# Optimization experiments

Hardware: AMD Instinct MI355X
Metric: run time of the kernel (lower is better)

The kernel has to match this reference:

```python
import jax, jax.numpy as jnp
import numpy as np

B, S, D = 512, 199, 128
PRO, SKILL = 20000, 500


def setup_inputs() -> dict:
    key = jax.random.key(0)
    ks = jax.random.split(key, 32)
    rn = lambda k, shape: jax.random.normal(k, shape, dtype=jnp.float32) * 0.05
    inp = {}
    inp["last_problem"] = jax.random.randint(ks[0], (B, S), 0, PRO, dtype=jnp.int32)
    inp["last_skill"] = jax.random.randint(ks[1], (B, S), 0, SKILL, dtype=jnp.int32)
    inp["last_ans"] = jax.random.randint(ks[2], (B, S), 0, 2, dtype=jnp.int32)
    inp["next_problem"] = jax.random.randint(ks[3], (B, S), 0, PRO, dtype=jnp.int32)
    inp["next_skill"] = jax.random.randint(ks[4], (B, S), 0, SKILL, dtype=jnp.int32)
    inp["next_ans"] = jax.random.randint(ks[5], (B, S), 0, 2, dtype=jnp.int32)
    inp["pro_embed"] = rn(ks[6], (PRO, D))
    inp["skill_embed"] = rn(ks[7], (SKILL, D))
    inp["ans_embed"] = rn(ks[8], (2, D))
    inp["time_embed"] = rn(ks[9], (200, D))
    inp["ls_state"] = rn(ks[10], (1, D))
    inp["pro_state0"] = rn(ks[11], (199, D))
    inp["skill_state0"] = rn(ks[12], (199, D))
    inp["akt_pro_diff"] = rn(ks[13], (PRO, 1))
    inp["akt_pro_change"] = rn(ks[14], (SKILL, D))
    # Linear weights stored as [in, out] (torch W.T); biases zero-init.
    inp["W_pf"] = rn(ks[15], (2 * D, D)); inp["b_pf"] = jnp.zeros((D,), jnp.float32)
    inp["W_sf"] = rn(ks[16], (2 * D, D)); inp["b_sf"] = jnp.zeros((D,), jnp.float32)
    inp["W_af"] = rn(ks[17], (2 * D, D)); inp["b_af"] = jnp.zeros((D,), jnp.float32)
    inp["W_ps"] = rn(ks[18], (2 * D, D)); inp["b_ps"] = jnp.zeros((D,), jnp.float32)
    inp["W_ss"] = rn(ks[19], (2 * D, D)); inp["b_ss"] = jnp.zeros((D,), jnp.float32)
    inp["W_as"] = rn(ks[20], (2 * D, D)); inp["b_as"] = jnp.zeros((D,), jnp.float32)
    inp["W_o1"] = rn(ks[21], (4 * D, D)); inp["b_o1"] = jnp.zeros((D,), jnp.float32)
    inp["W_o2"] = rn(ks[22], (D, 1));     inp["b_o2"] = jnp.zeros((1,), jnp.float32)
    return inp


def _forward(next_problem, next_skill, next_ans,
             pro_embed, skill_embed, ans_embed, time_embed, ls_state,
             pro_state0, skill_state0, akt_pro_diff, akt_pro_change,
             W_pf, b_pf, W_sf, b_sf, W_af, b_af,
             W_ps, b_ps, W_ss, b_ss, W_as, b_as,
             W_o1, b_o1, W_o2, b_o2):
    Bb, Ss = next_problem.shape
    Dd = pro_embed.shape[1]
    # [B,S,D] question embedding with AKT-style difficulty modulation
    npe = (pro_embed[next_problem] + skill_embed[next_skill]
           + akt_pro_diff[next_problem] * akt_pro_change[next_skill])
    nX = npe + ans_embed[next_ans]
    atge = time_embed[1]  # all_time_gap == 1 every step
    bidx = jnp.arange(Bb)

    def step(carry, x):
        pro_state, skill_state, all_state, lpt_tab, lst_tab = carry
        t, npe_t, nX_t, pidx, sidx = x
        # gather last-seen states via per-batch time indices
        lpt = lpt_tab[bidx, pidx]               # [B] int
        lbp = pro_state[bidx, lpt]              # [B,D]
        tge = time_embed[t - lpt]               # [B,D]
        lst = lst_tab[bidx, sidx]
        lbs = skill_state[bidx, lst]
        stge = time_embed[t - lst]
        # forget gates
        lbp = lbp * jax.nn.sigmoid(jnp.concatenate([lbp, tge], -1) @ W_pf + b_pf)
        lbs = lbs * jax.nn.sigmoid(jnp.concatenate([lbs, stge], -1) @ W_sf + b_sf)
        atge_b = jnp.broadcast_to(atge, all_state.shape)
        la = all_state * jax.nn.sigmoid(jnp.concatenate([all_state, atge_b], -1) @ W_af + b_af)
        # prediction head
        final = jnp.concatenate([la, lbp, lbs, npe_t], -1)  # [B,4D]
        P = jax.nn.sigmoid(jax.nn.relu(final @ W_o1 + b_o1) @ W_o2 + b_o2)[:, 0]
        # state updates
        new_all = la + jnp.tanh(jnp.concatenate([la, nX_t], -1) @ W_as + b_as)
        new_pro = lbp + jnp.tanh(jnp.concatenate([lbp, nX_t], -1) @ W_ps + b_ps)
        new_skill = lbs + jnp.tanh(jnp.concatenate([lbs, nX_t], -1) @ W_ss + b_ss)
        # scatter time and state back
        lpt_tab = lpt_tab.at[bidx, pidx].set(t)
        lst_tab = lst_tab.at[bidx, sidx].set(t)
        pro_state = jax.lax.dynamic_update_slice_in_dim(pro_state, new_pro[:, None, :], t, axis=1)
        skill_state = jax.lax.dynamic_update_slice_in_dim(skill_state, new_skill[:, None, :], t, axis=1)
        return (pro_state, skill_state, new_all, lpt_tab, lst_tab), P

    init = (jnp.broadcast_to(pro_state0[None], (Bb, pro_state0.shape[0], Dd)),
            jnp.broadcast_to(skill_state0[None], (Bb, skill_state0.shape[0], Dd)),
            jnp.broadcast_to(ls_state, (Bb, Dd)),
            jnp.zeros((Bb, akt_pro_diff.shape[0]), jnp.int32),
            jnp.zeros((Bb, akt_pro_change.shape[0]), jnp.int32))
    xs = (jnp.arange(Ss, dtype=jnp.int32),
          jnp.swapaxes(npe, 0, 1), jnp.swapaxes(nX, 0, 1),
          next_problem.T, next_skill.T)
    _, Ps = jax.lax.scan(step, init, xs)  # Ps: [S,B]
    return Ps.T  # [B,S]


def reference(last_problem, last_skill, last_ans, next_problem, next_skill, next_ans,
              pro_embed, skill_embed, ans_embed, time_embed, ls_state,
              pro_state0, skill_state0, akt_pro_diff, akt_pro_change,
              W_pf, b_pf, W_sf, b_sf, W_af, b_af,
              W_ps, b_ps, W_ss, b_ss, W_as, b_as,
              W_o1, b_o1, W_o2, b_o2):
    # last_problem/last_skill/last_ans are only used for shape in the original forward
    return _forward(next_problem, next_skill, next_ans,
                    pro_embed, skill_embed, ans_embed, time_embed, ls_state,
                    pro_state0, skill_state0, akt_pro_diff, akt_pro_change,
                    W_pf, b_pf, W_sf, b_sf, W_af, b_af,
                    W_ps, b_ps, W_ss, b_ss, W_as, b_as,
                    W_o1, b_o1, W_o2, b_o2)
```

## Files before the change

kernel.cpp:

```cpp
#include <hip/hip_runtime.h>
#include <hip/hip_bf16.h>

typedef __bf16 bf16;
typedef bf16 bf16x8 __attribute__((ext_vector_type(8)));
typedef bf16 bf16x4 __attribute__((ext_vector_type(4)));
typedef float f32x4 __attribute__((ext_vector_type(4)));
typedef unsigned int u32;
typedef unsigned short u16;

#define Bsz 512
#define Ssz 199
#define Dsz 128
#define GR 16
#define NBLK (Bsz / GR)
#define BTot (Bsz * Ssz)

__device__ __forceinline__ float fsig(float x) {
  return __builtin_amdgcn_rcpf(1.f + __builtin_amdgcn_exp2f(x * -1.44269504f));
}
__device__ __forceinline__ float ftanh(float x) {
  return 1.f - 2.f * __builtin_amdgcn_rcpf(1.f + __builtin_amdgcn_exp2f(x * 2.88539008f));
}
__device__ __forceinline__ f32x4 mfma16(bf16x8 a, bf16x8 b, f32x4 c) {
  return __builtin_amdgcn_mfma_f32_16x16x32_bf16(a, b, c, 0, 0, 0);
}
__device__ __forceinline__ bf16x8 ldfrag(const bf16* PW, int KS, int nt, int ks, int lane) {
  return *(const bf16x8*)&PW[(size_t)((nt * KS + ks) * 64 + lane) * 8];
}
__device__ __forceinline__ void keep(bf16x8& v) {
  f32x4& f = reinterpret_cast<f32x4&>(v);
  asm volatile("" : "+v"(f));
}
__device__ __forceinline__ void barL() {
  __builtin_amdgcn_sched_barrier(0);
  asm volatile("s_waitcnt lgkmcnt(0)" ::: "memory");
  __builtin_amdgcn_s_barrier();
  __builtin_amdgcn_sched_barrier(0);
}

__global__ void k_idx(const int* __restrict__ np_, const int* __restrict__ ns_,
                      u32* __restrict__ idx) {
  __shared__ u16 tabP[20000];
  __shared__ u16 tabS[500];
  __shared__ u16 pb[Ssz], sb[Ssz];
  int b = blockIdx.x;
  for (int i = threadIdx.x; i < 20000; i += blockDim.x) tabP[i] = 0;
  for (int i = threadIdx.x; i < 500; i += blockDim.x) tabS[i] = 0;
  for (int i = threadIdx.x; i < Ssz; i += blockDim.x) {
    pb[i] = (u16)np_[b * Ssz + i];
    sb[i] = (u16)ns_[b * Ssz + i];
  }
  __syncthreads();
  if (threadIdx.x == 0) {
    for (int t = 0; t < Ssz; ++t) {
      int p = pb[t], s = sb[t];
      idx[b * Ssz + t] = (u32)tabP[p] | ((u32)tabS[s] << 8);
      tabP[p] = (u16)t;
      tabS[s] = (u16)t;
    }
  }
}

__global__ void k_pack(const float* __restrict__ W, bf16* __restrict__ dst, int K) {
  int g = blockIdx.x * blockDim.x + threadIdx.x;
  int KS = K / 32;
  int total = 8 * KS * 64;
  if (g >= total) return;
  int l = g & 63;
  int ks = (g >> 6) % KS;
  int nt = (g >> 6) / KS;
  int col = nt * 16 + (l & 15);
  int k0 = ks * 32 + (l >> 4) * 8;
  bf16x8 v;
  for (int j = 0; j < 8; ++j) v[j] = (bf16)W[(size_t)(k0 + j) * 128 + col];
  *(bf16x8*)&dst[(size_t)g * 8] = v;
}

__global__ void k_tge(const float* __restrict__ TE, const float* __restrict__ W,
                      const float* __restrict__ bias, float* __restrict__ dst) {
  __shared__ float te[128];
  int d = blockIdx.x, n = threadIdx.x;
  te[n] = TE[d * 128 + n];
  __syncthreads();
  float acc = bias[n];
  for (int k = 0; k < 128; ++k) acc += te[k] * W[(size_t)(128 + k) * 128 + n];
  dst[d * 128 + n] = acc;
}

__global__ void k_embed(const int* __restrict__ np_, const int* __restrict__ ns_,
                        const int* __restrict__ na_,
                        const float* __restrict__ pe, const float* __restrict__ se,
                        const float* __restrict__ diff, const float* __restrict__ chg,
                        const float* __restrict__ ae, bf16* __restrict__ nXsS) {
  int g = blockIdx.x * 256 + threadIdx.x;
  int bt = g >> 5, cg = (g & 31) * 4;
  if (bt >= BTot) return;
  int b = bt / Ssz, t = bt - b * Ssz;
  int p = np_[bt], s = ns_[bt], a = na_[bt];
  float d = diff[p];
  f32x4 vp = *(const f32x4*)&pe[(size_t)p * 128 + cg];
  f32x4 vs = *(const f32x4*)&se[(size_t)s * 128 + cg];
  f32x4 vc = *(const f32x4*)&chg[(size_t)s * 128 + cg];
  f32x4 va = *(const f32x4*)&ae[(size_t)a * 128 + cg];
  bf16x4 ox;
  for (int j = 0; j < 4; ++j) ox[j] = (bf16)(vp[j] + vs[j] + d * vc[j] + va[j]);
  *(bf16x4*)&nXsS[((size_t)t * Bsz + b) * 128 + cg] = ox;
}

struct MainParams {
  const float *ls_state, *pro_state0, *skill_state0;
  const u32 *idx;
  const bf16 *nXsS;
  const float *TGEp, *TGEs, *cAF;
  const bf16 *PWpf, *PWsf, *PWaf, *PWps, *PWss, *PWas;
  const float *b_ps, *b_ss, *b_as;
  bf16 *proSt, *skSt, *Sla, *Slbp, *Slbs;
};

__global__ void __launch_bounds__(512) k_main(MainParams P) {
  const int b0 = blockIdx.x * GR;
  const int tid = threadIdx.x;
  const int lane = tid & 63;
  const int wv = tid >> 6;
  const int r32 = tid >> 5;
  const int c4 = (tid & 31) * 4;
  const int arow = lane & 15, apos = (lane >> 4) * 8;
  const int rb = (lane >> 4) * 4;
  const int cA = wv * 16 + (lane & 15);

  __shared__ __align__(16) bf16 Ala[16][136], Albp[16][136], Albs[16][136], AnX[16][136];
  __shared__ __align__(16) bf16 STG0[16][132], STG1[16][132], STGa[16][132];
  __shared__ u32 idxL[GR * Ssz];

  bf16x8 Wpf[4], Wsf[4], Waf[4], Wps[8], Wss[8], Was[8];
#pragma unroll
  for (int ks = 0; ks < 4; ++ks) {
    Wpf[ks] = ldfrag(P.PWpf, 4, wv, ks, lane);
    Wsf[ks] = ldfrag(P.PWsf, 4, wv, ks, lane);
    Waf[ks] = ldfrag(P.PWaf, 4, wv, ks, lane);
  }
#pragma unroll
  for (int ks = 0; ks < 8; ++ks) {
    Wps[ks] = ldfrag(P.PWps, 8, wv, ks, lane);
    Wss[ks] = ldfrag(P.PWss, 8, wv, ks, lane);
    Was[ks] = ldfrag(P.PWas, 8, wv, ks, lane);
  }
#pragma unroll
  for (int ks = 0; ks < 4; ++ks) {
    keep(Wpf[ks]);
    keep(Wsf[ks]);
    keep(Waf[ks]);
  }
#pragma unroll
  for (int ks = 0; ks < 8; ++ks) {
    keep(Wps[ks]);
    keep(Wss[ks]);
    keep(Was[ks]);
  }
  const float bpsv = P.b_ps[cA], bssv = P.b_ss[cA], basv = P.b_as[cA], cafv = P.cAF[cA];

  for (int i = tid; i < GR * Ssz; i += 512) idxL[i] = P.idx[b0 * Ssz + i];
  __syncthreads();

  float gpc[4], gsc[4];
  {
    bf16x4 va, vp, vs;
    for (int j = 0; j < 4; ++j) {
      va[j] = (bf16)P.ls_state[c4 + j];
      vp[j] = (bf16)P.pro_state0[c4 + j];
      vs[j] = (bf16)P.skill_state0[c4 + j];
    }
    *(bf16x4*)&Ala[r32][c4] = va;
    *(bf16x4*)&Albp[r32][c4] = vp;
    *(bf16x4*)&Albs[r32][c4] = vs;
    *(bf16x4*)&AnX[r32][c4] = *(const bf16x4*)&P.nXsS[(size_t)(b0 + r32) * Dsz + c4];
#pragma unroll
    for (int r = 0; r < 4; ++r) {
      gpc[r] = P.TGEp[cA];
      gsc[r] = P.TGEs[cA];
    }
  }
  __syncthreads();

  for (int t = 0; t < Ssz; ++t) {
    const bool pf = (t + 1 < Ssz);
    float gpn[4], gsn[4];
    bf16x4 pPro{}, pSk{}, pNxs{};
    u32 iwN = 0;
    if (pf) {
#pragma unroll
      for (int r = 0; r < 4; ++r) {
        u32 iw = idxL[(rb + r) * Ssz + t + 1];
        int lp = iw & 255, ls = (iw >> 8) & 255;
        gpn[r] = P.TGEp[(size_t)(t + 1 - lp) * Dsz + cA];
        gsn[r] = P.TGEs[(size_t)(t + 1 - ls) * Dsz + cA];
      }
      iwN = idxL[r32 * Ssz + t + 1];
      int lpN = iwN & 255, lsN = (iwN >> 8) & 255;
      if (lpN != t)
        pPro = *(const bf16x4*)&P.proSt[((size_t)(b0 + r32) * Ssz + lpN) * Dsz + c4];
      if (lsN != t)
        pSk = *(const bf16x4*)&P.skSt[((size_t)(b0 + r32) * Ssz + lsN) * Dsz + c4];
      pNxs = *(const bf16x4*)&P.nXsS[((size_t)(t + 1) * Bsz + (b0 + r32)) * Dsz + c4];
    }
    f32x4 dpf = {gpc[0], gpc[1], gpc[2], gpc[3]};
    f32x4 dsf = {gsc[0], gsc[1], gsc[2], gsc[3]};
    f32x4 daf = {cafv, cafv, cafv, cafv};
#pragma unroll
    for (int ks = 0; ks < 4; ++ks) {
      bf16x8 ap = *(const bf16x8*)&Albp[arow][ks * 32 + apos];
      bf16x8 av = *(const bf16x8*)&Albs[arow][ks * 32 + apos];
      bf16x8 aa = *(const bf16x8*)&Ala[arow][ks * 32 + apos];
      dpf = mfma16(ap, Wpf[ks], dpf);
      dsf = mfma16(av, Wsf[ks], dsf);
      daf = mfma16(aa, Waf[ks], daf);
    }
    barL();
    float gP[4], gS[4], gA[4];
#pragma unroll
    for (int r = 0; r < 4; ++r) {
      int row = rb + r;
      float sp = (float)Albp[row][cA];
      float gv = sp * fsig(dpf[r]);
      gP[r] = gv;
      Albp[row][cA] = (bf16)gv;
      float ss = (float)Albs[row][cA];
      float gw = ss * fsig(dsf[r]);
      gS[r] = gw;
      Albs[row][cA] = (bf16)gw;
      float sa = (float)Ala[row][cA];
      float gx = sa * fsig(daf[r]);
      gA[r] = gx;
      Ala[row][cA] = (bf16)gx;
    }
    barL();
    {
      size_t db = ((size_t)(b0 + r32) * Ssz + t) * Dsz + c4;
      *(bf16x4*)&P.Sla[db] = *(const bf16x4*)&Ala[r32][c4];
      *(bf16x4*)&P.Slbp[db] = *(const bf16x4*)&Albp[r32][c4];
      *(bf16x4*)&P.Slbs[db] = *(const bf16x4*)&Albs[r32][c4];
    }
    f32x4 uas{}, ups{}, uss{};
#pragma unroll
    for (int ks = 0; ks < 4; ++ks) {
      bf16x8 aa = *(const bf16x8*)&Ala[arow][ks * 32 + apos];
      bf16x8 ap = *(const bf16x8*)&Albp[arow][ks * 32 + apos];
      bf16x8 av = *(const bf16x8*)&Albs[arow][ks * 32 + apos];
      bf16x8 ax = *(const bf16x8*)&AnX[arow][ks * 32 + apos];
      uas = mfma16(aa, Was[ks], uas);
      uas = mfma16(ax, Was[ks + 4], uas);
      ups = mfma16(ap, Wps[ks], ups);
      ups = mfma16(ax, Wps[ks + 4], ups);
      uss = mfma16(av, Wss[ks], uss);
      uss = mfma16(ax, Wss[ks + 4], uss);
    }
#pragma unroll
    for (int r = 0; r < 4; ++r) {
      int row = rb + r;
      STG0[row][cA] = (bf16)(gP[r] + ftanh(ups[r] + bpsv));
      STG1[row][cA] = (bf16)(gS[r] + ftanh(uss[r] + bssv));
      STGa[row][cA] = (bf16)(gA[r] + ftanh(uas[r] + basv));
    }
    barL();
    {
      size_t base = ((size_t)(b0 + r32) * Ssz + t) * Dsz + c4;
      bf16x4 npv = *(const bf16x4*)&STG0[r32][c4];
      bf16x4 nsv = *(const bf16x4*)&STG1[r32][c4];
      *(bf16x4*)&P.proSt[base] = npv;
      *(bf16x4*)&P.skSt[base] = nsv;
      if (pf) {
        int lpN = iwN & 255, lsN = (iwN >> 8) & 255;
        *(bf16x4*)&Ala[r32][c4] = *(const bf16x4*)&STGa[r32][c4];
        *(bf16x4*)&Albp[r32][c4] = (lpN == t) ? npv : pPro;
        *(bf16x4*)&Albs[r32][c4] = (lsN == t) ? nsv : pSk;
        *(bf16x4*)&AnX[r32][c4] = pNxs;
#pragma unroll
        for (int r = 0; r < 4; ++r) {
          gpc[r] = gpn[r];
          gsc[r] = gsn[r];
        }
      }
    }
    __syncthreads();
  }
}

struct HeadParams {
  const bf16 *Sla, *Slbp, *Slbs, *PWo1;
  const int *next_problem, *next_skill;
  const float *pro_embed, *skill_embed, *akt_pro_diff, *akt_pro_change;
  const float *b_o1, *W_o2, *b_o2;
  float *out;
};

__global__ void k_head(HeadParams P) {
  const int bt0 = blockIdx.x * 32;
  const int tid = threadIdx.x, lane = tid & 63, wv = tid >> 6;
  const int r16 = tid >> 4, c8 = (tid & 15) * 8;
  const int arow = lane & 15, apos = (lane >> 4) * 8;
  const int rb = (lane >> 4) * 4;
  const int nt0 = wv, nt1 = wv + 4;
  const int cAh = nt0 * 16 + (lane & 15), cBh = nt1 * 16 + (lane & 15);
  __shared__ __align__(16) bf16 Af[32][520];
  __shared__ float Hh[32][132];
  __shared__ float Hpart[32][16];
  __shared__ float w2s[128];
  if (tid < 128) w2s[tid] = P.W_o2[tid];
  for (int half = 0; half < 2; ++half) {
    int row = half * 16 + r16;
    int bt = bt0 + row;
    *(bf16x8*)&Af[row][c8] = *(const bf16x8*)&P.Sla[(size_t)bt * 128 + c8];
    *(bf16x8*)&Af[row][128 + c8] = *(const bf16x8*)&P.Slbp[(size_t)bt * 128 + c8];
    *(bf16x8*)&Af[row][256 + c8] = *(const bf16x8*)&P.Slbs[(size_t)bt * 128 + c8];
    int np = P.next_problem[bt], ns = P.next_skill[bt];
    float diff = P.akt_pro_diff[np];
    f32x4 p0 = *(const f32x4*)&P.pro_embed[(size_t)np * 128 + c8];
    f32x4 p1 = *(const f32x4*)&P.pro_embed[(size_t)np * 128 + c8 + 4];
    f32x4 s0 = *(const f32x4*)&P.skill_embed[(size_t)ns * 128 + c8];
    f32x4 s1 = *(const f32x4*)&P.skill_embed[(size_t)ns * 128 + c8 + 4];
    f32x4 c0 = *(const f32x4*)&P.akt_pro_change[(size_t)ns * 128 + c8];
    f32x4 c1 = *(const f32x4*)&P.akt_pro_change[(size_t)ns * 128 + c8 + 4];
    bf16x8 vn;
    for (int j = 0; j < 4; ++j) {
      vn[j] = (bf16)(p0[j] + s0[j] + diff * c0[j]);
      vn[j + 4] = (bf16)(p1[j] + s1[j] + diff * c1[j]);
    }
    *(bf16x8*)&Af[row][384 + c8] = vn;
  }
  __syncthreads();
  f32x4 h0{}, h1{}, h2{}, h3{};
#pragma unroll
  for (int ks = 0; ks < 16; ++ks) {
    bf16x8 a0 = *(const bf16x8*)&Af[arow][ks * 32 + apos];
    bf16x8 a1 = *(const bf16x8*)&Af[16 + arow][ks * 32 + apos];
    bf16x8 bA = ldfrag(P.PWo1, 16, nt0, ks, lane);
    bf16x8 bB = ldfrag(P.PWo1, 16, nt1, ks, lane);
    h0 = mfma16(a0, bA, h0);
    h1 = mfma16(a0, bB, h1);
    h2 = mfma16(a1, bA, h2);
    h3 = mfma16(a1, bB, h3);
  }
  const float bo1A = P.b_o1[cAh], bo1B = P.b_o1[cBh];
  for (int r = 0; r < 4; ++r) {
    Hh[rb + r][cAh] = fmaxf(h0[r] + bo1A, 0.f);
    Hh[rb + r][cBh] = fmaxf(h1[r] + bo1B, 0.f);
    Hh[16 + rb + r][cAh] = fmaxf(h2[r] + bo1A, 0.f);
    Hh[16 + rb + r][cBh] = fmaxf(h3[r] + bo1B, 0.f);
  }
  __syncthreads();
  for (int half = 0; half < 2; ++half) {
    int row = half * 16 + (tid >> 4), cg = tid & 15;
    float s = 0.f;
#pragma unroll
    for (int j = 0; j < 8; ++j) s += Hh[row][cg * 8 + j] * w2s[cg * 8 + j];
    Hpart[row][cg] = s;
  }
  __syncthreads();
  if (tid < 32) {
    float s = 0.f;
#pragma unroll
    for (int k = 0; k < 16; ++k) s += Hpart[tid][k];
    P.out[bt0 + tid] = fsig(s + P.b_o2[0]);
  }
}

extern "C" void kernel_launch(void* const* d_in, const int* in_sizes, int n_in,
                              void* d_out, int out_size, void* d_ws, size_t ws_size,
                              hipStream_t stream) {
  const int* next_problem = (const int*)d_in[3];
  const int* next_skill = (const int*)d_in[4];
  const int* next_ans = (const int*)d_in[5];
  const float* pro_embed = (const float*)d_in[6];
  const float* skill_embed = (const float*)d_in[7];
  const float* ans_embed = (const float*)d_in[8];
  const float* time_embed = (const float*)d_in[9];
  const float* ls_state = (const float*)d_in[10];
  const float* pro_state0 = (const float*)d_in[11];
  const float* skill_state0 = (const float*)d_in[12];
  const float* akt_pro_diff = (const float*)d_in[13];
  const float* akt_pro_change = (const float*)d_in[14];
  const float* W_pf = (const float*)d_in[15];
  const float* b_pf = (const float*)d_in[16];
  const float* W_sf = (const float*)d_in[17];
  const float* b_sf = (const float*)d_in[18];
  const float* W_af = (const float*)d_in[19];
  const float* b_af = (const float*)d_in[20];
  const float* W_ps = (const float*)d_in[21];
  const float* b_ps = (const float*)d_in[22];
  const float* W_ss = (const float*)d_in[23];
  const float* b_ss = (const float*)d_in[24];
  const float* W_as = (const float*)d_in[25];
  const float* b_as = (const float*)d_in[26];
  const float* W_o1 = (const float*)d_in[27];
  const float* b_o1 = (const float*)d_in[28];
  const float* W_o2 = (const float*)d_in[29];
  const float* b_o2 = (const float*)d_in[30];

  char* ws = (char*)d_ws;
  size_t off = 0;
  auto alloc = [&](size_t bytes) -> void* {
    void* p = ws + off;
    off += bytes;
    off = (off + 255) & ~(size_t)255;
    return p;
  };
  bf16* proSt = (bf16*)alloc((size_t)Bsz * Ssz * Dsz * 2);
  bf16* skSt = (bf16*)alloc((size_t)Bsz * Ssz * Dsz * 2);
  u32* idx = (u32*)alloc((size_t)BTot * 4);
  float* TGEp = (float*)alloc(200 * 128 * 4);
  float* TGEs = (float*)alloc(200 * 128 * 4);
  float* cAF = (float*)alloc(128 * 4);
  bf16* PWpf = (bf16*)alloc(128 * 128 * 2);
  bf16* PWsf = (bf16*)alloc(128 * 128 * 2);
  bf16* PWaf = (bf16*)alloc(128 * 128 * 2);
  bf16* PWps = (bf16*)alloc(256 * 128 * 2);
  bf16* PWss = (bf16*)alloc(256 * 128 * 2);
  bf16* PWas = (bf16*)alloc(256 * 128 * 2);
  bf16* PWo1 = (bf16*)alloc(512 * 128 * 2);
  bf16* nXsS = (bf16*)alloc((size_t)BTot * Dsz * 2);
  bf16* Sla = (bf16*)alloc((size_t)BTot * Dsz * 2);
  bf16* Slbp = (bf16*)alloc((size_t)BTot * Dsz * 2);
  bf16* Slbs = (bf16*)alloc((size_t)BTot * Dsz * 2);

  if (off > ws_size) {
    hipMemsetAsync(d_out, 0xFF, (size_t)out_size * 4, stream);
    return;
  }

  k_idx<<<Bsz, 256, 0, stream>>>(next_problem, next_skill, idx);
  k_pack<<<8, 256, 0, stream>>>(W_pf, PWpf, 128);
  k_pack<<<8, 256, 0, stream>>>(W_sf, PWsf, 128);
  k_pack<<<8, 256, 0, stream>>>(W_af, PWaf, 128);
  k_pack<<<16, 256, 0, stream>>>(W_ps, PWps, 256);
  k_pack<<<16, 256, 0, stream>>>(W_ss, PWss, 256);
  k_pack<<<16, 256, 0, stream>>>(W_as, PWas, 256);
  k_pack<<<32, 256, 0, stream>>>(W_o1, PWo1, 512);
  k_tge<<<200, 128, 0, stream>>>(time_embed, W_pf, b_pf, TGEp);
  k_tge<<<200, 128, 0, stream>>>(time_embed, W_sf, b_sf, TGEs);
  k_tge<<<1, 128, 0, stream>>>(time_embed + 128, W_af, b_af, cAF);
  k_embed<<<(BTot * 32 + 255) / 256, 256, 0, stream>>>(
      next_problem, next_skill, next_ans, pro_embed, skill_embed, akt_pro_diff,
      akt_pro_change, ans_embed, nXsS);

  MainParams mp;
  mp.ls_state = ls_state; mp.pro_state0 = pro_state0; mp.skill_state0 = skill_state0;
  mp.idx = idx;
  mp.nXsS = nXsS;
  mp.TGEp = TGEp; mp.TGEs = TGEs; mp.cAF = cAF;
  mp.PWpf = PWpf; mp.PWsf = PWsf; mp.PWaf = PWaf;
  mp.PWps = PWps; mp.PWss = PWss; mp.PWas = PWas;
  mp.b_ps = b_ps; mp.b_ss = b_ss; mp.b_as = b_as;
  mp.proSt = proSt; mp.skSt = skSt;
  mp.Sla = Sla; mp.Slbp = Slbp; mp.Slbs = Slbs;

  k_main<<<NBLK, 512, 0, stream>>>(mp);

  HeadParams hp;
  hp.Sla = Sla; hp.Slbp = Slbp; hp.Slbs = Slbs; hp.PWo1 = PWo1;
  hp.next_problem = next_problem; hp.next_skill = next_skill;
  hp.pro_embed = pro_embed; hp.skill_embed = skill_embed;
  hp.akt_pro_diff = akt_pro_diff; hp.akt_pro_change = akt_pro_change;
  hp.b_o1 = b_o1; hp.W_o2 = W_o2; hp.b_o2 = b_o2;
  hp.out = (float*)d_out;
  k_head<<<BTot / 32, 256, 0, stream>>>(hp);
}
```

Measured before the change: 715.7 us.

## Double-buffer recurrent state in LDS and defer global stores by one step

```diff
diff --git a/kernel.cpp b/kernel.cpp
--- a/kernel.cpp
+++ b/kernel.cpp
@@ -128,8 +128,9 @@
   const int rb = (lane >> 4) * 4;
   const int cA = wv * 16 + (lane & 15);
 
-  __shared__ __align__(16) bf16 Ala[16][136], Albp[16][136], Albs[16][136], AnX[16][136];
-  __shared__ __align__(16) bf16 STG0[16][132], STG1[16][132], STGa[16][132];
+  __shared__ __align__(16) bf16 Ala[2][16][136], Albp[2][16][136], Albs[2][16][136];
+  __shared__ __align__(16) bf16 AnX[2][16][136];
+  __shared__ __align__(16) bf16 STG0[2][16][132], STG1[2][16][132], STGa[16][132];
   __shared__ u32 idxL[GR * Ssz];
 
   bf16x8 Wpf[4], Wsf[4], Waf[4], Wps[8], Wss[8], Was[8];
@@ -170,10 +171,10 @@
       vp[j] = (bf16)P.pro_state0[c4 + j];
       vs[j] = (bf16)P.skill_state0[c4 + j];
     }
-    *(bf16x4*)&Ala[r32][c4] = va;
-    *(bf16x4*)&Albp[r32][c4] = vp;
-    *(bf16x4*)&Albs[r32][c4] = vs;
-    *(bf16x4*)&AnX[r32][c4] = *(const bf16x4*)&P.nXsS[(size_t)(b0 + r32) * Dsz + c4];
+    *(bf16x4*)&Ala[0][r32][c4] = va;
+    *(bf16x4*)&Albp[0][r32][c4] = vp;
+    *(bf16x4*)&Albs[0][r32][c4] = vs;
+    *(bf16x4*)&AnX[0][r32][c4] = *(const bf16x4*)&P.nXsS[(size_t)(b0 + r32) * Dsz + c4];
 #pragma unroll
     for (int r = 0; r < 4; ++r) {
       gpc[r] = P.TGEp[cA];
@@ -184,9 +185,18 @@
 
   for (int t = 0; t < Ssz; ++t) {
     const bool pf = (t + 1 < Ssz);
+    const int cur = t & 1, prv = cur ^ 1;
+    if (t > 0) {
+      size_t sb = ((size_t)(b0 + r32) * Ssz + (t - 1)) * Dsz + c4;
+      *(bf16x4*)&P.proSt[sb] = *(const bf16x4*)&STG0[prv][r32][c4];
+      *(bf16x4*)&P.skSt[sb] = *(const bf16x4*)&STG1[prv][r32][c4];
+      *(bf16x4*)&P.Sla[sb] = *(const bf16x4*)&Ala[prv][r32][c4];
+      *(bf16x4*)&P.Slbp[sb] = *(const bf16x4*)&Albp[prv][r32][c4];
+      *(bf16x4*)&P.Slbs[sb] = *(const bf16x4*)&Albs[prv][r32][c4];
+    }
     float gpn[4], gsn[4];
     bf16x4 pPro{}, pSk{}, pNxs{};
-    u32 iwN = 0;
+    int lpN = 0, lsN = 0;
     if (pf) {
 #pragma unroll
       for (int r = 0; r < 4; ++r) {
@@ -195,11 +205,12 @@
         gpn[r] = P.TGEp[(size_t)(t + 1 - lp) * Dsz + cA];
         gsn[r] = P.TGEs[(size_t)(t + 1 - ls) * Dsz + cA];
       }
-      iwN = idxL[r32 * Ssz + t + 1];
-      int lpN = iwN & 255, lsN = (iwN >> 8) & 255;
-      if (lpN != t)
+      u32 iwN = idxL[r32 * Ssz + t + 1];
+      lpN = iwN & 255;
+      lsN = (iwN >> 8) & 255;
+      if (lpN < t - 1)
         pPro = *(const bf16x4*)&P.proSt[((size_t)(b0 + r32) * Ssz + lpN) * Dsz + c4];
-      if (lsN != t)
+      if (lsN < t - 1)
         pSk = *(const bf16x4*)&P.skSt[((size_t)(b0 + r32) * Ssz + lsN) * Dsz + c4];
       pNxs = *(const bf16x4*)&P.nXsS[((size_t)(t + 1) * Bsz + (b0 + r32)) * Dsz + c4];
     }
@@ -208,9 +219,9 @@
     f32x4 daf = {cafv, cafv, cafv, cafv};
 #pragma unroll
     for (int ks = 0; ks < 4; ++ks) {
-      bf16x8 ap = *(const bf16x8*)&Albp[arow][ks * 32 + apos];
-      bf16x8 av = *(const bf16x8*)&Albs[arow][ks * 32 + apos];
-      bf16x8 aa = *(const bf16x8*)&Ala[arow][ks * 32 + apos];
+      bf16x8 ap = *(const bf16x8*)&Albp[cur][arow][ks * 32 + apos];
+      bf16x8 av = *(const bf16x8*)&Albs[cur][arow][ks * 32 + apos];
+      bf16x8 aa = *(const bf16x8*)&Ala[cur][arow][ks * 32 + apos];
       dpf = mfma16(ap, Wpf[ks], dpf);
       dsf = mfma16(av, Wsf[ks], dsf);
       daf = mfma16(aa, Waf[ks], daf);
@@ -220,33 +231,24 @@
 #pragma unroll
     for (int r = 0; r < 4; ++r) {
       int row = rb + r;
-      float sp = (float)Albp[row][cA];
-      float gv = sp * fsig(dpf[r]);
+      float gv = (float)Albp[cur][row][cA] * fsig(dpf[r]);
       gP[r] = gv;
-      Albp[row][cA] = (bf16)gv;
-      float ss = (float)Albs[row][cA];
-      float gw = ss * fsig(dsf[r]);
+      Albp[cur][row][cA] = (bf16)gv;
+      float gw = (float)Albs[cur][row][cA] * fsig(dsf[r]);
       gS[r] = gw;
-      Albs[row][cA] = (bf16)gw;
-      float sa = (float)Ala[row][cA];
-      float gx = sa * fsig(daf[r]);
+      Albs[cur][row][cA] = (bf16)gw;
+      float gx = (float)Ala[cur][row][cA] * fsig(daf[r]);
       gA[r] = gx;
-      Ala[row][cA] = (bf16)gx;
+      Ala[cur][row][cA] = (bf16)gx;
     }
     barL();
-    {
-      size_t db = ((size_t)(b0 + r32) * Ssz + t) * Dsz + c4;
-      *(bf16x4*)&P.Sla[db] = *(const bf16x4*)&Ala[r32][c4];
-      *(bf16x4*)&P.Slbp[db] = *(const bf16x4*)&Albp[r32][c4];
-      *(bf16x4*)&P.Slbs[db] = *(const bf16x4*)&Albs[r32][c4];
-    }
     f32x4 uas{}, ups{}, uss{};
 #pragma unroll
     for (int ks = 0; ks < 4; ++ks) {
-      bf16x8 aa = *(const bf16x8*)&Ala[arow][ks * 32 + apos];
-      bf16x8 ap = *(const bf16x8*)&Albp[arow][ks * 32 + apos];
-      bf16x8 av = *(const bf16x8*)&Albs[arow][ks * 32 + apos];
-      bf16x8 ax = *(const bf16x8*)&AnX[arow][ks * 32 + apos];
+      bf16x8 aa = *(const bf16x8*)&Ala[cur][arow][ks * 32 + apos];
+      bf16x8 ap = *(const bf16x8*)&Albp[cur][arow][ks * 32 + apos];
+      bf16x8 av = *(const bf16x8*)&Albs[cur][arow][ks * 32 + apos];
+      bf16x8 ax = *(const bf16x8*)&AnX[cur][arow][ks * 32 + apos];
       uas = mfma16(aa, Was[ks], uas);
       uas = mfma16(ax, Was[ks + 4], uas);
       ups = mfma16(ap, Wps[ks], ups);
@@ -257,31 +259,39 @@
 #pragma unroll
     for (int r = 0; r < 4; ++r) {
       int row = rb + r;
-      STG0[row][cA] = (bf16)(gP[r] + ftanh(ups[r] + bpsv));
-      STG1[row][cA] = (bf16)(gS[r] + ftanh(uss[r] + bssv));
+      STG0[cur][row][cA] = (bf16)(gP[r] + ftanh(ups[r] + bpsv));
+      STG1[cur][row][cA] = (bf16)(gS[r] + ftanh(uss[r] + bssv));
       STGa[row][cA] = (bf16)(gA[r] + ftanh(uas[r] + basv));
     }
     barL();
-    {
-      size_t base = ((size_t)(b0 + r32) * Ssz + t) * Dsz + c4;
-      bf16x4 npv = *(const bf16x4*)&STG0[r32][c4];
-      bf16x4 nsv = *(const bf16x4*)&STG1[r32][c4];
-      *(bf16x4*)&P.proSt[base] = npv;
-      *(bf16x4*)&P.skSt[base] = nsv;
-      if (pf) {
-        int lpN = iwN & 255, lsN = (iwN >> 8) & 255;
-        *(bf16x4*)&Ala[r32][c4] = *(const bf16x4*)&STGa[r32][c4];
-        *(bf16x4*)&Albp[r32][c4] = (lpN == t) ? npv : pPro;
-        *(bf16x4*)&Albs[r32][c4] = (lsN == t) ? nsv : pSk;
-        *(bf16x4*)&AnX[r32][c4] = pNxs;
-#pragma unroll
-        for (int r = 0; r < 4; ++r) {
-          gpc[r] = gpn[r];
-          gsc[r] = gsn[r];
-        }
+    if (pf) {
+      const int nxt = cur ^ 1;
+      *(bf16x4*)&Ala[nxt][r32][c4] = *(const bf16x4*)&STGa[r32][c4];
+      bf16x4 ncur = *(const bf16x4*)&STG0[cur][r32][c4];
+      bf16x4 nprv = *(const bf16x4*)&STG0[prv][r32][c4];
+      *(bf16x4*)&Albp[nxt][r32][c4] =
+          (lpN == t) ? ncur : ((lpN == t - 1) ? nprv : pPro);
+      ncur = *(const bf16x4*)&STG1[cur][r32][c4];
+      nprv = *(const bf16x4*)&STG1[prv][r32][c4];
+      *(bf16x4*)&Albs[nxt][r32][c4] =
+          (lsN == t) ? ncur : ((lsN == t - 1) ? nprv : pSk);
+      *(bf16x4*)&AnX[nxt][r32][c4] = pNxs;
+#pragma unroll
+      for (int r = 0; r < 4; ++r) {
+        gpc[r] = gpn[r];
+        gsc[r] = gsn[r];
       }
     }
     __syncthreads();
+  }
+  {
+    const int last = (Ssz - 1) & 1;
+    size_t sb = ((size_t)(b0 + r32) * Ssz + (Ssz - 1)) * Dsz + c4;
+    *(bf16x4*)&P.proSt[sb] = *(const bf16x4*)&STG0[last][r32][c4];
+    *(bf16x4*)&P.skSt[sb] = *(const bf16x4*)&STG1[last][r32][c4];
+    *(bf16x4*)&P.Sla[sb] = *(const bf16x4*)&Ala[last][r32][c4];
+    *(bf16x4*)&P.Slbp[sb] = *(const bf16x4*)&Albp[last][r32][c4];
+    *(bf16x4*)&P.Slbs[sb] = *(const bf16x4*)&Albs[last][r32][c4];
   }
 }
 
```

Result: slower. 743.5 us (+3.9%).

## Interleave two 16-row batch groups per block in skewed software pipeline

Applied to the files above, without the earlier changes.

```diff
diff --git a/kernel.cpp b/kernel.cpp
--- a/kernel.cpp
+++ b/kernel.cpp
@@ -11,8 +11,8 @@
 #define Bsz 512
 #define Ssz 199
 #define Dsz 128
-#define GR 16
-#define NBLK (Bsz / GR)
+#define GR2 32
+#define NBLK2 (Bsz / GR2)
 #define BTot (Bsz * Ssz)
 
 __device__ __forceinline__ float fsig(float x) {
@@ -118,7 +118,7 @@
 };
 
 __global__ void __launch_bounds__(512) k_main(MainParams P) {
-  const int b0 = blockIdx.x * GR;
+  const int b0 = blockIdx.x * GR2;
   const int tid = threadIdx.x;
   const int lane = tid & 63;
   const int wv = tid >> 6;
@@ -128,9 +128,10 @@
   const int rb = (lane >> 4) * 4;
   const int cA = wv * 16 + (lane & 15);
 
-  __shared__ __align__(16) bf16 Ala[16][136], Albp[16][136], Albs[16][136], AnX[16][136];
-  __shared__ __align__(16) bf16 STG0[16][132], STG1[16][132], STGa[16][132];
-  __shared__ u32 idxL[GR * Ssz];
+  __shared__ __align__(16) bf16 Ala[2][16][140], Albp[2][16][140], Albs[2][16][140];
+  __shared__ __align__(16) bf16 AnX[2][16][140];
+  __shared__ __align__(16) bf16 SP[2][2][16][132], SS[2][2][16][132], SA[2][16][132];
+  __shared__ u32 idxL[GR2 * Ssz];
 
   bf16x8 Wpf[4], Wsf[4], Waf[4], Wps[8], Wss[8], Was[8];
 #pragma unroll
@@ -159,10 +160,10 @@
   }
   const float bpsv = P.b_ps[cA], bssv = P.b_ss[cA], basv = P.b_as[cA], cafv = P.cAF[cA];
 
-  for (int i = tid; i < GR * Ssz; i += 512) idxL[i] = P.idx[b0 * Ssz + i];
-  __syncthreads();
-
-  float gpc[4], gsc[4];
+  for (int i = tid; i < GR2 * Ssz; i += 512) idxL[i] = P.idx[b0 * Ssz + i];
+  __syncthreads();
+
+  float gpc0[4], gsc0[4], gpc1[4], gsc1[4];
   {
     bf16x4 va, vp, vs;
     for (int j = 0; j < 4; ++j) {
@@ -170,118 +171,230 @@
       vp[j] = (bf16)P.pro_state0[c4 + j];
       vs[j] = (bf16)P.skill_state0[c4 + j];
     }
-    *(bf16x4*)&Ala[r32][c4] = va;
-    *(bf16x4*)&Albp[r32][c4] = vp;
-    *(bf16x4*)&Albs[r32][c4] = vs;
-    *(bf16x4*)&AnX[r32][c4] = *(const bf16x4*)&P.nXsS[(size_t)(b0 + r32) * Dsz + c4];
+#pragma unroll
+    for (int g = 0; g < 2; ++g) {
+      *(bf16x4*)&Ala[g][r32][c4] = va;
+      *(bf16x4*)&Albp[g][r32][c4] = vp;
+      *(bf16x4*)&Albs[g][r32][c4] = vs;
+      *(bf16x4*)&AnX[g][r32][c4] =
+          *(const bf16x4*)&P.nXsS[(size_t)(b0 + g * 16 + r32) * Dsz + c4];
+    }
 #pragma unroll
     for (int r = 0; r < 4; ++r) {
-      gpc[r] = P.TGEp[cA];
-      gsc[r] = P.TGEs[cA];
-    }
-  }
-  __syncthreads();
+      gpc0[r] = P.TGEp[cA];
+      gsc0[r] = P.TGEs[cA];
+      gpc1[r] = gpc0[r];
+      gsc1[r] = gsc0[r];
+    }
+  }
+  __syncthreads();
+
+  f32x4 uas1{}, ups1{}, uss1{};
+  float gP1[4], gS1[4], gA1[4];
+  bf16x4 pPro1{}, pSk1{}, pNxs1{};
+  int lpN1 = 0, lsN1 = 0;
+  float gpn1P[4], gpn1S[4];
 
   for (int t = 0; t < Ssz; ++t) {
     const bool pf = (t + 1 < Ssz);
-    float gpn[4], gsn[4];
-    bf16x4 pPro{}, pSk{}, pNxs{};
-    u32 iwN = 0;
+    const int cb = t & 1, pb = cb ^ 1;
+    float gpn0P[4], gpn0S[4];
+    bf16x4 pPro0{}, pSk0{}, pNxs0{};
+    int lpN0 = 0, lsN0 = 0;
     if (pf) {
 #pragma unroll
       for (int r = 0; r < 4; ++r) {
         u32 iw = idxL[(rb + r) * Ssz + t + 1];
         int lp = iw & 255, ls = (iw >> 8) & 255;
-        gpn[r] = P.TGEp[(size_t)(t + 1 - lp) * Dsz + cA];
-        gsn[r] = P.TGEs[(size_t)(t + 1 - ls) * Dsz + cA];
+        gpn0P[r] = P.TGEp[(size_t)(t + 1 - lp) * Dsz + cA];
+        gpn0S[r] = P.TGEs[(size_t)(t + 1 - ls) * Dsz + cA];
       }
-      iwN = idxL[r32 * Ssz + t + 1];
-      int lpN = iwN & 255, lsN = (iwN >> 8) & 255;
-      if (lpN != t)
-        pPro = *(const bf16x4*)&P.proSt[((size_t)(b0 + r32) * Ssz + lpN) * Dsz + c4];
-      if (lsN != t)
-        pSk = *(const bf16x4*)&P.skSt[((size_t)(b0 + r32) * Ssz + lsN) * Dsz + c4];
-      pNxs = *(const bf16x4*)&P.nXsS[((size_t)(t + 1) * Bsz + (b0 + r32)) * Dsz + c4];
-    }
-    f32x4 dpf = {gpc[0], gpc[1], gpc[2], gpc[3]};
-    f32x4 dsf = {gsc[0], gsc[1], gsc[2], gsc[3]};
-    f32x4 daf = {cafv, cafv, cafv, cafv};
+      u32 iw = idxL[r32 * Ssz + t + 1];
+      lpN0 = iw & 255;
+      lsN0 = (iw >> 8) & 255;
+      if (lpN0 != t)
+        pPro0 = *(const bf16x4*)&P.proSt[((size_t)(b0 + r32) * Ssz + lpN0) * Dsz + c4];
+      if (lsN0 != t)
+        pSk0 = *(const bf16x4*)&P.skSt[((size_t)(b0 + r32) * Ssz + lsN0) * Dsz + c4];
+      pNxs0 = *(const bf16x4*)&P.nXsS[((size_t)(t + 1) * Bsz + (b0 + r32)) * Dsz + c4];
+    }
+    f32x4 dpf0 = {gpc0[0], gpc0[1], gpc0[2], gpc0[3]};
+    f32x4 dsf0 = {gsc0[0], gsc0[1], gsc0[2], gsc0[3]};
+    f32x4 daf0 = {cafv, cafv, cafv, cafv};
 #pragma unroll
     for (int ks = 0; ks < 4; ++ks) {
-      bf16x8 ap = *(const bf16x8*)&Albp[arow][ks * 32 + apos];
-      bf16x8 av = *(const bf16x8*)&Albs[arow][ks * 32 + apos];
-      bf16x8 aa = *(const bf16x8*)&Ala[arow][ks * 32 + apos];
-      dpf = mfma16(ap, Wpf[ks], dpf);
-      dsf = mfma16(av, Wsf[ks], dsf);
-      daf = mfma16(aa, Waf[ks], daf);
+      bf16x8 ap = *(const bf16x8*)&Albp[0][arow][ks * 32 + apos];
+      bf16x8 av = *(const bf16x8*)&Albs[0][arow][ks * 32 + apos];
+      bf16x8 aa = *(const bf16x8*)&Ala[0][arow][ks * 32 + apos];
+      dpf0 = mfma16(ap, Wpf[ks], dpf0);
+      dsf0 = mfma16(av, Wsf[ks], dsf0);
+      daf0 = mfma16(aa, Waf[ks], daf0);
+    }
+    if (t > 0) {
+#pragma unroll
+      for (int r = 0; r < 4; ++r) {
+        int row = rb + r;
+        SA[1][row][cA] = (bf16)(gA1[r] + ftanh(uas1[r] + basv));
+        SP[1][pb][row][cA] = (bf16)(gP1[r] + ftanh(ups1[r] + bpsv));
+        SS[1][pb][row][cA] = (bf16)(gS1[r] + ftanh(uss1[r] + bssv));
+      }
     }
     barL();
-    float gP[4], gS[4], gA[4];
+    float gP0[4], gS0[4], gA0[4];
 #pragma unroll
     for (int r = 0; r < 4; ++r) {
       int row = rb + r;
-      float sp = (float)Albp[row][cA];
-      float gv = sp * fsig(dpf[r]);
-      gP[r] = gv;
-      Albp[row][cA] = (bf16)gv;
-      float ss = (float)Albs[row][cA];
-      float gw = ss * fsig(dsf[r]);
-      gS[r] = gw;
-      Albs[row][cA] = (bf16)gw;
-      float sa = (float)Ala[row][cA];
-      float gx = sa * fsig(daf[r]);
-      gA[r] = gx;
-      Ala[row][cA] = (bf16)gx;
+      float gv = (float)Albp[0][row][cA] * fsig(dpf0[r]);
+      gP0[r] = gv;
+      Albp[0][row][cA] = (bf16)gv;
+      float gw = (float)Albs[0][row][cA] * fsig(dsf0[r]);
+      gS0[r] = gw;
+      Albs[0][row][cA] = (bf16)gw;
+      float gx = (float)Ala[0][row][cA] * fsig(daf0[r]);
+      gA0[r] = gx;
+      Ala[0][row][cA] = (bf16)gx;
+    }
+    if (t > 0) {
+      size_t sb = ((size_t)(b0 + 16 + r32) * Ssz + (t - 1)) * Dsz + c4;
+      bf16x4 npv = *(const bf16x4*)&SP[1][pb][r32][c4];
+      bf16x4 nsv = *(const bf16x4*)&SS[1][pb][r32][c4];
+      *(bf16x4*)&P.proSt[sb] = npv;
+      *(bf16x4*)&P.skSt[sb] = nsv;
+      *(bf16x4*)&P.Sla[sb] = *(const bf16x4*)&Ala[1][r32][c4];
+      *(bf16x4*)&P.Slbp[sb] = *(const bf16x4*)&Albp[1][r32][c4];
+      *(bf16x4*)&P.Slbs[sb] = *(const bf16x4*)&Albs[1][r32][c4];
+      *(bf16x4*)&Ala[1][r32][c4] = *(const bf16x4*)&SA[1][r32][c4];
+      bf16x4 old = *(const bf16x4*)&SP[1][cb][r32][c4];
+      *(bf16x4*)&Albp[1][r32][c4] =
+          (lpN1 == t - 1) ? npv : ((lpN1 == t - 2) ? old : pPro1);
+      old = *(const bf16x4*)&SS[1][cb][r32][c4];
+      *(bf16x4*)&Albs[1][r32][c4] =
+          (lsN1 == t - 1) ? nsv : ((lsN1 == t - 2) ? old : pSk1);
+      *(bf16x4*)&AnX[1][r32][c4] = pNxs1;
+#pragma unroll
+      for (int r = 0; r < 4; ++r) {
+        gpc1[r] = gpn1P[r];
+        gsc1[r] = gpn1S[r];
+      }
+    }
+    barL();
+    if (pf) {
+#pragma unroll
+      for (int r = 0; r < 4; ++r) {
+        u32 iw = idxL[(16 + rb + r) * Ssz + t + 1];
+        int lp = iw & 255, ls = (iw >> 8) & 255;
+        gpn1P[r] = P.TGEp[(size_t)(t + 1 - lp) * Dsz + cA];
+        gpn1S[r] = P.TGEs[(size_t)(t + 1 - ls) * Dsz + cA];
+      }
+      u32 iw = idxL[(16 + r32) * Ssz + t + 1];
+      lpN1 = iw & 255;
+      lsN1 = (iw >> 8) & 255;
+      pPro1 = bf16x4{};
+      pSk1 = bf16x4{};
+      if (lpN1 < t - 1)
+        pPro1 =
+            *(const bf16x4*)&P.proSt[((size_t)(b0 + 16 + r32) * Ssz + lpN1) * Dsz + c4];
+      if (lsN1 < t - 1)
+        pSk1 =
+            *(const bf16x4*)&P.skSt[((size_t)(b0 + 16 + r32) * Ssz + lsN1) * Dsz + c4];
+      pNxs1 =
+          *(const bf16x4*)&P.nXsS[((size_t)(t + 1) * Bsz + (b0 + 16 + r32)) * Dsz + c4];
+    }
+    f32x4 uas0{}, ups0{}, uss0{};
+    f32x4 dpf1 = {gpc1[0], gpc1[1], gpc1[2], gpc1[3]};
+    f32x4 dsf1 = {gsc1[0], gsc1[1], gsc1[2], gsc1[3]};
+    f32x4 daf1 = {cafv, cafv, cafv, cafv};
+#pragma unroll
+    for (int ks = 0; ks < 4; ++ks) {
+      bf16x8 aa = *(const bf16x8*)&Ala[0][arow][ks * 32 + apos];
+      bf16x8 ap = *(const bf16x8*)&Albp[0][arow][ks * 32 + apos];
+      bf16x8 av = *(const bf16x8*)&Albs[0][arow][ks * 32 + apos];
+      bf16x8 ax = *(const bf16x8*)&AnX[0][arow][ks * 32 + apos];
+      uas0 = mfma16(aa, Was[ks], uas0);
+      uas0 = mfma16(ax, Was[ks + 4], uas0);
+      ups0 = mfma16(ap, Wps[ks], ups0);
+      ups0 = mfma16(ax, Wps[ks + 4], ups0);
+      uss0 = mfma16(av, Wss[ks], uss0);
+      uss0 = mfma16(ax, Wss[ks + 4], uss0);
+      bf16x8 bp = *(const bf16x8*)&Albp[1][arow][ks * 32 + apos];
+      bf16x8 bv = *(const bf16x8*)&Albs[1][arow][ks * 32 + apos];
+      bf16x8 ba = *(const bf16x8*)&Ala[1][arow][ks * 32 + apos];
+      dpf1 = mfma16(bp, Wpf[ks], dpf1);
+      dsf1 = mfma16(bv, Wsf[ks], dsf1);
+      daf1 = mfma16(ba, Waf[ks], daf1);
+    }
+    barL();
+#pragma unroll
+    for (int r = 0; r < 4; ++r) {
+      int row = rb + r;
+      SA[0][row][cA] = (bf16)(gA0[r] + ftanh(uas0[r] + basv));
+      SP[0][cb][row][cA] = (bf16)(gP0[r] + ftanh(ups0[r] + bpsv));
+      SS[0][cb][row][cA] = (bf16)(gS0[r] + ftanh(uss0[r] + bssv));
+      float gv = (float)Albp[1][row][cA] * fsig(dpf1[r]);
+      gP1[r] = gv;
+      Albp[1][row][cA] = (bf16)gv;
+      float gw = (float)Albs[1][row][cA] * fsig(dsf1[r]);
+      gS1[r] = gw;
+      Albs[1][row][cA] = (bf16)gw;
+      float gx = (float)Ala[1][row][cA] * fsig(daf1[r]);
+      gA1[r] = gx;
+      Ala[1][row][cA] = (bf16)gx;
     }
     barL();
     {
-      size_t db = ((size_t)(b0 + r32) * Ssz + t) * Dsz + c4;
-      *(bf16x4*)&P.Sla[db] = *(const bf16x4*)&Ala[r32][c4];
-      *(bf16x4*)&P.Slbp[db] = *(const bf16x4*)&Albp[r32][c4];
-      *(bf16x4*)&P.Slbs[db] = *(const bf16x4*)&Albs[r32][c4];
-    }
-    f32x4 uas{}, ups{}, uss{};
+      size_t sb = ((size_t)(b0 + r32) * Ssz + t) * Dsz + c4;
+      bf16x4 npv = *(const bf16x4*)&SP[0][cb][r32][c4];
+      bf16x4 nsv = *(const bf16x4*)&SS[0][cb][r32][c4];
+      *(bf16x4*)&P.proSt[sb] = npv;
+      *(bf16x4*)&P.skSt[sb] = nsv;
+      *(bf16x4*)&P.Sla[sb] = *(const bf16x4*)&Ala[0][r32][c4];
+      *(bf16x4*)&P.Slbp[sb] = *(const bf16x4*)&Albp[0][r32][c4];
+      *(bf16x4*)&P.Slbs[sb] = *(const bf16x4*)&Albs[0][r32][c4];
+      if (pf) {
+        *(bf16x4*)&Ala[0][r32][c4] = *(const bf16x4*)&SA[0][r32][c4];
+        *(bf16x4*)&Albp[0][r32][c4] = (lpN0 == t) ? npv : pPro0;
+        *(bf16x4*)&Albs[0][r32][c4] = (lsN0 == t) ? nsv : pSk0;
+        *(bf16x4*)&AnX[0][r32][c4] = pNxs0;
+#pragma unroll
+        for (int r = 0; r < 4; ++r) {
+          gpc0[r] = gpn0P[r];
+          gsc0[r] = gpn0S[r];
+        }
+      }
+    }
+    uas1 = f32x4{};
+    ups1 = f32x4{};
+    uss1 = f32x4{};
 #pragma unroll
     for (int ks = 0; ks < 4; ++ks) {
-      bf16x8 aa = *(const bf16x8*)&Ala[arow][ks * 32 + apos];
-      bf16x8 ap = *(const bf16x8*)&Albp[arow][ks * 32 + apos];
-      bf16x8 av = *(const bf16x8*)&Albs[arow][ks * 32 + apos];
-      bf16x8 ax = *(const bf16x8*)&AnX[arow][ks * 32 + apos];
-      uas = mfma16(aa, Was[ks], uas);
-      uas = mfma16(ax, Was[ks + 4], uas);
-      ups = mfma16(ap, Wps[ks], ups);
-      ups = mfma16(ax, Wps[ks + 4], ups);
-      uss = mfma16(av, Wss[ks], uss);
-      uss = mfma16(ax, Wss[ks + 4], uss);
-    }
+      bf16x8 aa = *(const bf16x8*)&Ala[1][arow][ks * 32 + apos];
+      bf16x8 ap = *(const bf16x8*)&Albp[1][arow][ks * 32 + apos];
+      bf16x8 av = *(const bf16x8*)&Albs[1][arow][ks * 32 + apos];
+      bf16x8 ax = *(const bf16x8*)&AnX[1][arow][ks * 32 + apos];
+      uas1 = mfma16(aa, Was[ks], uas1);
+      uas1 = mfma16(ax, Was[ks + 4], uas1);
+      ups1 = mfma16(ap, Wps[ks], ups1);
+      ups1 = mfma16(ax, Wps[ks + 4], ups1);
+      uss1 = mfma16(av, Wss[ks], uss1);
+      uss1 = mfma16(ax, Wss[ks + 4], uss1);
+    }
+    __syncthreads();
+  }
+  {
+    const int fb = (Ssz - 1) & 1;
 #pragma unroll
     for (int r = 0; r < 4; ++r) {
       int row = rb + r;
-      STG0[row][cA] = (bf16)(gP[r] + ftanh(ups[r] + bpsv));
-      STG1[row][cA] = (bf16)(gS[r] + ftanh(uss[r] + bssv));
-      STGa[row][cA] = (bf16)(gA[r] + ftanh(uas[r] + basv));
+      SP[1][fb][row][cA] = (bf16)(gP1[r] + ftanh(ups1[r] + bpsv));
+      SS[1][fb][row][cA] = (bf16)(gS1[r] + ftanh(uss1[r] + bssv));
     }
     barL();
-    {
-      size_t base = ((size_t)(b0 + r32) * Ssz + t) * Dsz + c4;
-      bf16x4 npv = *(const bf16x4*)&STG0[r32][c4];
-      bf16x4 nsv = *(const bf16x4*)&STG1[r32][c4];
-      *(bf16x4*)&P.proSt[base] = npv;
-      *(bf16x4*)&P.skSt[base] = nsv;
-      if (pf) {
-        int lpN = iwN & 255, lsN = (iwN >> 8) & 255;
-        *(bf16x4*)&Ala[r32][c4] = *(const bf16x4*)&STGa[r32][c4];
-        *(bf16x4*)&Albp[r32][c4] = (lpN == t) ? npv : pPro;
-        *(bf16x4*)&Albs[r32][c4] = (lsN == t) ? nsv : pSk;
-        *(bf16x4*)&AnX[r32][c4] = pNxs;
-#pragma unroll
-        for (int r = 0; r < 4; ++r) {
-          gpc[r] = gpn[r];
-          gsc[r] = gsn[r];
-        }
-      }
-    }
-    __syncthreads();
+    size_t sb = ((size_t)(b0 + 16 + r32) * Ssz + (Ssz - 1)) * Dsz + c4;
+    *(bf16x4*)&P.proSt[sb] = *(const bf16x4*)&SP[1][fb][r32][c4];
+    *(bf16x4*)&P.skSt[sb] = *(const bf16x4*)&SS[1][fb][r32][c4];
+    *(bf16x4*)&P.Sla[sb] = *(const bf16x4*)&Ala[1][r32][c4];
+    *(bf16x4*)&P.Slbp[sb] = *(const bf16x4*)&Albp[1][r32][c4];
+    *(bf16x4*)&P.Slbs[sb] = *(const bf16x4*)&Albs[1][r32][c4];
   }
 }
 
@@ -453,7 +566,7 @@
   mp.proSt = proSt; mp.skSt = skSt;
   mp.Sla = Sla; mp.Slbp = Slbp; mp.Slbs = Slbs;
 
-  k_main<<<NBLK, 512, 0, stream>>>(mp);
+  k_main<<<NBLK2, 512, 0, stream>>>(mp);
 
   HeadParams hp;
   hp.Sla = Sla; hp.Slbp = Slbp; hp.Slbs = Slbs; hp.PWo1 = PWo1;
```

New measurement: 2.261 ms. +215.9%, slower.
